# Optimization experiments

Measured on AMD Instinct MI355X. Metric: run time of the kernel, lower is better.

## Reference

```python
import jax, jax.numpy as jnp
import numpy as np

HEADS = 16
D_MODEL = 1024
D_K = D_MODEL // HEADS


def setup_inputs() -> dict:
    key = jax.random.key(0)
    ks = jax.random.split(key, 11)
    B, S, D = 4, 2048, D_MODEL
    q = jax.random.normal(ks[0], (B, S, D), dtype=jnp.float32)
    k = jax.random.normal(ks[1], (B, S, D), dtype=jnp.float32)
    v = jax.random.normal(ks[2], (B, S, D), dtype=jnp.float32)
    s = 1.0 / np.sqrt(D)
    Wq = jax.random.normal(ks[3], (D, D), dtype=jnp.float32) * s
    bq = jax.random.normal(ks[4], (D,), dtype=jnp.float32) * 0.01
    Wk = jax.random.normal(ks[5], (D, D), dtype=jnp.float32) * s
    bk = jax.random.normal(ks[6], (D,), dtype=jnp.float32) * 0.01
    Wv = jax.random.normal(ks[7], (D, D), dtype=jnp.float32) * s
    bv = jax.random.normal(ks[8], (D,), dtype=jnp.float32) * 0.01
    Wo = jax.random.normal(ks[9], (D, D), dtype=jnp.float32) * s
    bo = jax.random.normal(ks[10], (D,), dtype=jnp.float32) * 0.01
    return {"q": q, "k": k, "v": v, "Wq": Wq, "bq": bq, "Wk": Wk, "bk": bk,
            "Wv": Wv, "bv": bv, "Wo": Wo, "bo": bo}


def reference(q, k, v, Wq, bq, Wk, bk, Wv, bv, Wo, bo):
    B, Sq, D = q.shape
    Sk = k.shape[1]
    # Linear projections (torch Linear: x @ W.T + b)
    q_ = (q @ Wq.T + bq).reshape(B, Sq, HEADS, D_K).transpose(0, 2, 1, 3)  # [B,H,Sq,Dk]
    k_ = (k @ Wk.T + bk).reshape(B, Sk, HEADS, D_K).transpose(0, 2, 1, 3)  # [B,H,Sk,Dk]
    v_ = (v @ Wv.T + bv).reshape(B, Sk, HEADS, D_K).transpose(0, 2, 1, 3)  # [B,H,Sk,Dk]
    scores = jnp.einsum("bhqd,bhkd->bhqk", q_, k_) / jnp.sqrt(jnp.float32(D_K))
    attn = jax.nn.softmax(scores, axis=-1)
    ctx = jnp.einsum("bhqk,bhkd->bhqd", attn, v_)  # [B,H,Sq,Dk]
    concat = ctx.transpose(0, 2, 1, 3).reshape(B, Sq, D)
    # dropout p=0 -> identity (eval)
    return concat @ Wo.T + bo
```

## Files before the change

### kernel.cpp

```cpp
#include <hip/hip_runtime.h>
#include <hip/hip_bf16.h>
#include <stdint.h>

typedef unsigned short u16;
typedef __attribute__((ext_vector_type(8))) short bf16x8;
typedef __attribute__((ext_vector_type(4))) float f32x4;
typedef __attribute__((ext_vector_type(16))) float f32x16;
typedef __attribute__((ext_vector_type(4))) int i32x4;

#define BATCH 4
#define HEADS 16
#define SEQ   2048
#define DMODEL 1024
#define DK    64
#define QSCALE (0.125f * 1.44269504088896340736f)

__device__ __forceinline__ u16 f2bf(float f) {
  __hip_bfloat16 h = __float2bfloat16(f);
  return *reinterpret_cast<u16*>(&h);
}

__device__ __forceinline__ int cvtpk(float a, float b) {
  int r;
  asm("v_cvt_pk_bf16_f32 %0, %1, %2" : "=v"(r) : "v"(a), "v"(b));
  return r;
}

__device__ __forceinline__ void plswap(int& a, int& b) {
  asm volatile("v_permlane32_swap_b32 %0, %1" : "+v"(a), "+v"(b));
}

__device__ __forceinline__ void gload_lds16(const u16* g, u16* l) {
  __builtin_amdgcn_global_load_lds((const __attribute__((address_space(1))) void*)g,
                                   (__attribute__((address_space(3))) void*)l, 16, 0, 0);
}

__device__ __forceinline__ void sbar() {
  asm volatile("" ::: "memory");
  __builtin_amdgcn_s_barrier();
  __builtin_amdgcn_sched_barrier(0);
}
#define WAITV(N)                                              \
  do {                                                        \
    asm volatile("s_waitcnt vmcnt(" #N ")" ::: "memory");     \
    __builtin_amdgcn_sched_barrier(0);                        \
  } while (0)

__global__ void cvt_w(const float* __restrict__ w0, const float* __restrict__ w1,
                      const float* __restrict__ w2, const float* __restrict__ w3,
                      u16* __restrict__ o0, u16* __restrict__ o1,
                      u16* __restrict__ o2, u16* __restrict__ o3) {
  const int sel = blockIdx.y;
  long i = ((long)blockIdx.x * blockDim.x + threadIdx.x) * 8;
  const float* in = (sel == 0) ? w0 : (sel == 1) ? w1 : (sel == 2) ? w2 : w3;
  u16* out = (sel == 0) ? o0 : (sel == 1) ? o1 : (sel == 2) ? o2 : o3;
  float4 a = *(const float4*)(in + i);
  float4 b = *(const float4*)(in + i + 4);
  i32x4 pk;
  pk[0] = cvtpk(a.x, a.y); pk[1] = cvtpk(a.z, a.w);
  pk[2] = cvtpk(b.x, b.y); pk[3] = cvtpk(b.z, b.w);
  *(i32x4*)(out + i) = pk;
}

__global__ __launch_bounds__(256, 4)
void gemm97_qkv(const float* __restrict__ qf, const float* __restrict__ kf,
                const float* __restrict__ vf, const u16* __restrict__ Wqb,
                const u16* __restrict__ Wkb, const u16* __restrict__ Wvb,
                const float* __restrict__ bq, const float* __restrict__ bk,
                const float* __restrict__ bv, u16* __restrict__ Qp,
                u16* __restrict__ Kp, u16* __restrict__ Vt) {
  __shared__ __align__(16) u16 smem[16384];
  u16* As = smem;
  u16* Bs = smem + 8192;
  const int K = DMODEL;
  const int tid = threadIdx.x;
  const int lane = tid & 63;
  const int w = tid >> 6;
  const int wm = w >> 1, wn = w & 1;
  const int lr = lane & 15, lg = lane >> 4;

  const int wg = blockIdx.y * 24 + blockIdx.x;
  const int swz = (wg & 7) * 192 + (wg >> 3);
  const int bcolg = swz % 24;
  const int brow = swz / 24;
  const int sel = bcolg >> 3;
  const int bcol = bcolg & 7;

  const float* Ag = ((sel == 0) ? qf : (sel == 1) ? kf : vf) + (size_t)(brow * 128) * K;
  const u16* Bg = ((sel == 0) ? Wqb : (sel == 1) ? Wkb : Wvb) + (size_t)(bcol * 128) * K;
  const float* bias = (sel == 0) ? bq : (sel == 1) ? bk : bv;

  const int r0_ = tid >> 2;
  const int cc_ = (tid & 3) * 8;

  f32x4 acc[4][4] = {};
  float4 areg[2][2];

  areg[0][0] = *(const float4*)(Ag + (size_t)r0_ * K + cc_);
  areg[0][1] = *(const float4*)(Ag + (size_t)r0_ * K + cc_ + 4);
  areg[1][0] = *(const float4*)(Ag + (size_t)(r0_ + 64) * K + cc_);
  areg[1][1] = *(const float4*)(Ag + (size_t)(r0_ + 64) * K + cc_ + 4);
#pragma unroll
  for (int j = 0; j < 2; j++) {
    i32x4 pk;
    pk[0] = cvtpk(areg[j][0].x, areg[j][0].y);
    pk[1] = cvtpk(areg[j][0].z, areg[j][0].w);
    pk[2] = cvtpk(areg[j][1].x, areg[j][1].y);
    pk[3] = cvtpk(areg[j][1].z, areg[j][1].w);
    *(i32x4*)(As + (tid + j * 256) * 8) = pk;
  }
  gload_lds16(Bg + (size_t)r0_ * K + cc_, Bs + tid * 8);
  gload_lds16(Bg + (size_t)(r0_ + 64) * K + cc_, Bs + (tid + 256) * 8);
  areg[0][0] = *(const float4*)(Ag + (size_t)r0_ * K + 32 + cc_);
  areg[0][1] = *(const float4*)(Ag + (size_t)r0_ * K + 32 + cc_ + 4);
  areg[1][0] = *(const float4*)(Ag + (size_t)(r0_ + 64) * K + 32 + cc_);
  areg[1][1] = *(const float4*)(Ag + (size_t)(r0_ + 64) * K + 32 + cc_ + 4);
  __syncthreads();

  const int NT = 32;
  for (int t = 0; t < NT; ++t) {
    const int p = t & 1;
    const u16* Ab = As + p * 4096;
    const u16* Bb = Bs + p * 4096;

    if (t + 1 < NT) {
      u16* Ad = As + (p ^ 1) * 4096;
#pragma unroll
      for (int j = 0; j < 2; j++) {
        i32x4 pk;
        pk[0] = cvtpk(areg[j][0].x, areg[j][0].y);
        pk[1] = cvtpk(areg[j][0].z, areg[j][0].w);
        pk[2] = cvtpk(areg[j][1].x, areg[j][1].y);
        pk[3] = cvtpk(areg[j][1].z, areg[j][1].w);
        *(i32x4*)(Ad + (tid + j * 256) * 8) = pk;
      }
      u16* Bd = Bs + (p ^ 1) * 4096;
      const int k1 = (t + 1) * 32;
      gload_lds16(Bg + (size_t)r0_ * K + k1 + cc_, Bd + tid * 8);
      gload_lds16(Bg + (size_t)(r0_ + 64) * K + k1 + cc_, Bd + (tid + 256) * 8);
      if (t + 2 < NT) {
        const int k2 = (t + 2) * 32;
        areg[0][0] = *(const float4*)(Ag + (size_t)r0_ * K + k2 + cc_);
        areg[0][1] = *(const float4*)(Ag + (size_t)r0_ * K + k2 + cc_ + 4);
        areg[1][0] = *(const float4*)(Ag + (size_t)(r0_ + 64) * K + k2 + cc_);
        areg[1][1] = *(const float4*)(Ag + (size_t)(r0_ + 64) * K + k2 + cc_ + 4);
      }
    }

    bf16x8 a[4], b[4];
#pragma unroll
    for (int i = 0; i < 4; i++)
      a[i] = *(const bf16x8*)&Ab[(wm * 64 + i * 16 + lr) * 32 + lg * 8];
#pragma unroll
    for (int j = 0; j < 4; j++)
      b[j] = *(const bf16x8*)&Bb[(wn * 64 + j * 16 + lr) * 32 + lg * 8];
    __builtin_amdgcn_s_setprio(1);
#pragma unroll
    for (int i = 0; i < 4; i++)
#pragma unroll
      for (int j = 0; j < 4; j++)
        acc[i][j] = __builtin_amdgcn_mfma_f32_16x16x32_bf16(a[i], b[j], acc[i][j], 0, 0, 0);
    __builtin_amdgcn_s_setprio(0);

    __syncthreads();
  }

  if (sel < 2) {
    u16* Cout = (sel == 0) ? Qp : Kp;
    const float oscale = (sel == 0) ? QSCALE : 1.f;
#pragma unroll
    for (int j = 0; j < 4; j++) {
      const int col = bcol * 128 + wn * 64 + j * 16 + lr;
      const float bv_ = bias[col];
#pragma unroll
      for (int i = 0; i < 4; i++) {
        const int row0 = brow * 128 + wm * 64 + i * 16 + lg * 4;
#pragma unroll
        for (int r = 0; r < 4; r++)
          Cout[(size_t)(row0 + r) * DMODEL + col] = f2bf((acc[i][j][r] + bv_) * oscale);
      }
    }
  } else {
    const int b = brow >> 4;
    const int s0 = (brow & 15) * 128;
    u16* tr = smem;
    __syncthreads();
#pragma unroll
    for (int j = 0; j < 4; j++) {
      const int col = wn * 64 + j * 16 + lr;
      const int xsw = (col & 7) << 3;
      const float bv_ = bias[bcol * 128 + col];
#pragma unroll
      for (int i = 0; i < 4; i++) {
        const int rr0 = wm * 64 + i * 16 + lg * 4;
#pragma unroll
        for (int pr = 0; pr < 2; pr++) {
          const float e0 = acc[i][j][pr * 2] + bv_;
          const float e1 = acc[i][j][pr * 2 + 1] + bv_;
          *(int*)&tr[col * 128 + ((rr0 + pr * 2) ^ xsw)] = cvtpk(e0, e1);
        }
      }
    }
    __syncthreads();
    const int col = tid >> 1;
    const int part = tid & 1;
    const int xsw = (col & 7) << 3;
    const int c = bcol * 128 + col;
    const int hh = c >> 6, dk = c & 63;
    u16* dst = Vt + (size_t)((b * 16 + hh) * 64 + dk) * SEQ + s0 + part * 64;
#pragma unroll
    for (int jj = 0; jj < 8; jj++) {
      bf16x8 vv = *(const bf16x8*)&tr[col * 128 + ((part * 64 + jj * 8) ^ xsw)];
      *(bf16x8*)(dst + jj * 8) = vv;
    }
  }
}

__device__ __forceinline__ void gemm_kloop(
    const u16* __restrict__ Ag, const u16* __restrict__ Bg,
    u16* As, u16* Bs, f32x4 acc[4][4],
    const int tid, const int wm, const int wn, const int lr, const int lg) {
  const int K = DMODEL;
  int arow[4], acolc[4], brow2[2], bcol2[2];
#pragma unroll
  for (int j = 0; j < 4; j++) {
    const int c = tid + j * 512;
    arow[j] = c >> 3;
    acolc[j] = ((c & 7) ^ (arow[j] & 7)) * 8;
  }
#pragma unroll
  for (int j = 0; j < 2; j++) {
    const int c = tid + j * 512;
    brow2[j] = c >> 3;
    bcol2[j] = ((c & 7) ^ (brow2[j] & 7)) * 8;
  }

#pragma unroll
  for (int j = 0; j < 4; j++)
    gload_lds16(Ag + (size_t)arow[j] * K + acolc[j], As + (tid + j * 512) * 8);
#pragma unroll
  for (int j = 0; j < 2; j++)
    gload_lds16(Bg + (size_t)brow2[j] * K + bcol2[j], Bs + (tid + j * 512) * 8);
#pragma unroll
  for (int j = 0; j < 4; j++)
    gload_lds16(Ag + (size_t)arow[j] * K + 64 + acolc[j], As + 16384 + (tid + j * 512) * 8);
#pragma unroll
  for (int j = 0; j < 2; j++)
    gload_lds16(Bg + (size_t)brow2[j] * K + 64 + bcol2[j], Bs + 8192 + (tid + j * 512) * 8);
  WAITV(6);
  sbar();

  int m = 0;
  for (int t = 0; t < 16; ++t) {
    u16* Ab = As + m * 16384;
    u16* Bb = Bs + (t & 1) * 8192;
    const int m2 = (m + 2 >= 3) ? m - 1 : m + 2;
    const int k1 = (t + 1) * 64;
    const int k2 = (t + 2) * 64;

    bf16x8 a[4], b[4];
#pragma unroll
    for (int i = 0; i < 4; i++) {
      const int r = wm * 64 + i * 16 + lr;
      a[i] = *(const bf16x8*)&Ab[r * 64 + ((lg ^ (r & 7)) * 8)];
    }
#pragma unroll
    for (int j = 0; j < 4; j++) {
      const int r = wn * 64 + j * 16 + lr;
      b[j] = *(const bf16x8*)&Bb[r * 64 + ((lg ^ (r & 7)) * 8)];
    }
    if (t + 1 < 16) {
      u16* Bd = Bs + ((t + 1) & 1) * 8192;
      gload_lds16(Bg + (size_t)brow2[0] * K + k1 + bcol2[0], Bd + tid * 8);
      gload_lds16(Bg + (size_t)brow2[1] * K + k1 + bcol2[1], Bd + (tid + 512) * 8);
    }
    if (t + 2 < 16) {
      u16* Ad = As + m2 * 16384;
      gload_lds16(Ag + (size_t)arow[0] * K + k2 + acolc[0], Ad + tid * 8);
      gload_lds16(Ag + (size_t)arow[1] * K + k2 + acolc[1], Ad + (tid + 512) * 8);
    }
    sbar();
    __builtin_amdgcn_s_setprio(1);
#pragma unroll
    for (int i = 0; i < 4; i++)
#pragma unroll
      for (int j = 0; j < 4; j++)
        acc[i][j] = __builtin_amdgcn_mfma_f32_16x16x32_bf16(a[i], b[j], acc[i][j], 0, 0, 0);
    __builtin_amdgcn_s_setprio(0);
    sbar();

#pragma unroll
    for (int i = 0; i < 4; i++) {
      const int r = wm * 64 + i * 16 + lr;
      a[i] = *(const bf16x8*)&Ab[r * 64 + (((4 + lg) ^ (r & 7)) * 8)];
    }
#pragma unroll
    for (int j = 0; j < 4; j++) {
      const int r = wn * 64 + j * 16 + lr;
      b[j] = *(const bf16x8*)&Bb[r * 64 + (((4 + lg) ^ (r & 7)) * 8)];
    }
    if (t + 2 < 16) {
      u16* Ad = As + m2 * 16384;
      gload_lds16(Ag + (size_t)arow[2] * K + k2 + acolc[2], Ad + (tid + 1024) * 8);
      gload_lds16(Ag + (size_t)arow[3] * K + k2 + acolc[3], Ad + (tid + 1536) * 8);
    }
    sbar();
    __builtin_amdgcn_s_setprio(1);
#pragma unroll
    for (int i = 0; i < 4; i++)
#pragma unroll
      for (int j = 0; j < 4; j++)
        acc[i][j] = __builtin_amdgcn_mfma_f32_16x16x32_bf16(a[i], b[j], acc[i][j], 0, 0, 0);
    __builtin_amdgcn_s_setprio(0);
    if (t < 14) {
      WAITV(4);
    } else {
      WAITV(0);
    }
    sbar();
    m = (m + 1 >= 3) ? 0 : m + 1;
  }
}

__global__ __launch_bounds__(512, 2)
void gemm8_bt(const u16* __restrict__ A, const u16* __restrict__ Bm,
              const float* __restrict__ bias, float* __restrict__ Cout) {
  __shared__ __align__(16) u16 smem[65536];
  u16* As = smem;
  u16* Bs = smem + 49152;
  const int tid = threadIdx.x;
  const int lane = tid & 63;
  const int w = tid >> 6;
  const int wm = w >> 1, wn = w & 1;
  const int lr = lane & 15, lg = lane >> 4;

  const int wg = blockIdx.y * 8 + blockIdx.x;
  const int swz = (wg & 7) * 32 + (wg >> 3);
  const int bcol = swz & 7;
  const int brow = swz >> 3;

  f32x4 acc[4][4] = {};
  gemm_kloop(A + (size_t)(brow * 256) * DMODEL, Bm + (size_t)(bcol * 128) * DMODEL,
             As, Bs, acc, tid, wm, wn, lr, lg);

#pragma unroll
  for (int j = 0; j < 4; j++) {
    const int col = bcol * 128 + wn * 64 + j * 16 + lr;
    const float bv_ = bias[col];
#pragma unroll
    for (int i = 0; i < 4; i++) {
      const int row0 = brow * 256 + wm * 64 + i * 16 + lg * 4;
#pragma unroll
      for (int r = 0; r < 4; r++)
        Cout[(size_t)(row0 + r) * DMODEL + col] = acc[i][j][r] + bv_;
    }
  }
}

__device__ __forceinline__ void pack_group(const float* p, int* pw) {
  int W0 = cvtpk(p[0], p[1]);
  int W1 = cvtpk(p[2], p[3]);
  int W2 = cvtpk(p[4], p[5]);
  int W3 = cvtpk(p[6], p[7]);
  plswap(W0, W2);
  plswap(W1, W3);
  pw[0] = W0; pw[1] = W1; pw[2] = W2; pw[3] = W3;
}

__global__ __launch_bounds__(256, 4)
void attn2(const u16* __restrict__ Qp, const u16* __restrict__ Kp,
           const u16* __restrict__ Vt, u16* __restrict__ ctx) {
  __shared__ __align__(16) u16 smem[16384];
  const int tid = threadIdx.x;
  const int lane = tid & 63, w = tid >> 6;
  const int hi = lane >> 5;
  const int l31 = lane & 31;

  const int wg = blockIdx.y * gridDim.x + blockIdx.x;
  const int swz = (wg & 7) * 128 + (wg >> 3);
  const int bh = swz >> 4;
  const int b = bh >> 4, h = bh & 15;
  const int q0 = (swz & 15) * 128 + w * 32;

  const u16* qrow = Qp + (size_t)(b * SEQ + q0 + l31) * DMODEL + h * DK + hi * 8;
  bf16x8 qf[4];
#pragma unroll
  for (int kk = 0; kk < 4; kk++) qf[kk] = *(const bf16x8*)(qrow + kk * 16);

  const int srow = tid >> 3;
  const int scb = tid & 7;
  const int scol = (scb ^ (srow & 7)) * 8;
  const u16* kp = Kp + (size_t)(b * SEQ + srow) * DMODEL + h * DK + scol;
  const u16* vp = Vt + (size_t)bh * DK * SEQ + (size_t)srow * SEQ + scol;

  const int ksw = (l31 & 7) << 3;

  f32x16 o0 = {}, o1 = {};
  float lacc[4] = {};
  const int NT = SEQ / 64;

  {
    u16* Kd = smem;
    u16* Vd = smem + 4096;
    gload_lds16(kp, Kd + tid * 8);
    gload_lds16(kp + 32 * DMODEL, Kd + tid * 8 + 2048);
    gload_lds16(vp, Vd + tid * 8);
    gload_lds16(vp + 32 * SEQ, Vd + tid * 8 + 2048);
    kp += 64 * DMODEL;
    vp += 64;
  }
  __syncthreads();

  for (int t = 0; t < NT; ++t) {
    const int p = t & 1;
    if (t + 1 < NT) {
      u16* Kd = smem + ((p ^ 1) << 13);
      u16* Vd = Kd + 4096;
      gload_lds16(kp, Kd + tid * 8);
      gload_lds16(kp + 32 * DMODEL, Kd + tid * 8 + 2048);
      gload_lds16(vp, Vd + tid * 8);
      gload_lds16(vp + 32 * SEQ, Vd + tid * 8 + 2048);
      kp += 64 * DMODEL;
      vp += 64;
    }

    const u16* Kc = smem + (p << 13);
    const u16* Vc = Kc + 4096;

    f32x16 st0 = {}, st1 = {};
    __builtin_amdgcn_s_setprio(1);
#pragma unroll
    for (int kk = 0; kk < 4; kk++) {
      const int slot = (((kk * 2 + hi) << 3) ^ ksw);
      bf16x8 k0 = *(const bf16x8*)&Kc[l31 * 64 + slot];
      bf16x8 k1 = *(const bf16x8*)&Kc[(l31 + 32) * 64 + slot];
      st0 = __builtin_amdgcn_mfma_f32_32x32x16_bf16(k0, qf[kk], st0, 0, 0, 0);
      st1 = __builtin_amdgcn_mfma_f32_32x32x16_bf16(k1, qf[kk], st1, 0, 0, 0);
    }
    __builtin_amdgcn_s_setprio(0);

#pragma unroll
    for (int i = 0; i < 16; i++) st0[i] = __builtin_amdgcn_exp2f(st0[i]);
#pragma unroll
    for (int i = 0; i < 16; i++) st1[i] = __builtin_amdgcn_exp2f(st1[i]);
    float ts[8];
#pragma unroll
    for (int i = 0; i < 8; i++) ts[i] = (st0[i] + st0[i + 8]) + (st1[i] + st1[i + 8]);
#pragma unroll
    for (int i = 0; i < 4; i++) lacc[i] += ts[i] + ts[i + 4];

    int pw[4][4];
    {
      float tmp[8];
#pragma unroll
      for (int i = 0; i < 8; i++) tmp[i] = st0[i];
      pack_group(tmp, pw[0]);
#pragma unroll
      for (int i = 0; i < 8; i++) tmp[i] = st0[i + 8];
      pack_group(tmp, pw[1]);
#pragma unroll
      for (int i = 0; i < 8; i++) tmp[i] = st1[i];
      pack_group(tmp, pw[2]);
#pragma unroll
      for (int i = 0; i < 8; i++) tmp[i] = st1[i + 8];
      pack_group(tmp, pw[3]);
    }

    __builtin_amdgcn_s_setprio(1);
#pragma unroll
    for (int c = 0; c < 4; c++) {
      i32x4 pwv;
      pwv[0] = pw[c][0]; pwv[1] = pw[c][1]; pwv[2] = pw[c][2]; pwv[3] = pw[c][3];
      bf16x8 pf = __builtin_bit_cast(bf16x8, pwv);
      const int slot = (((c * 2 + hi) << 3) ^ ksw);
      bf16x8 v0 = *(const bf16x8*)&Vc[l31 * 64 + slot];
      bf16x8 v1 = *(const bf16x8*)&Vc[(l31 + 32) * 64 + slot];
      o0 = __builtin_amdgcn_mfma_f32_32x32x16_bf16(v0, pf, o0, 0, 0, 0);
      o1 = __builtin_amdgcn_mfma_f32_32x32x16_bf16(v1, pf, o1, 0, 0, 0);
    }
    __builtin_amdgcn_s_setprio(0);

    __syncthreads();
  }

  float lsum = (lacc[0] + lacc[1]) + (lacc[2] + lacc[3]);
  lsum += __shfl_xor(lsum, 32);
  const float rl = 1.0f / lsum;
  u16* ot = smem + w * (32 * 72);
#pragma unroll
  for (int ds_ = 0; ds_ < 2; ds_++) {
#pragma unroll
    for (int g = 0; g < 4; g++) {
#pragma unroll
      for (int pr = 0; pr < 2; pr++) {
        const int r = g * 4 + pr * 2;
        const int d = ds_ * 32 + (r & 3) + 8 * (r >> 2) + 4 * hi;
        float e0 = (ds_ ? o1[r] : o0[r]) * rl;
        float e1 = (ds_ ? o1[r + 1] : o0[r + 1]) * rl;
        *(int*)&ot[l31 * 72 + d] = cvtpk(e0, e1);
      }
    }
  }
  __syncthreads();
  const int rq = lane >> 3;
  const int rc = (lane & 7) * 8;
#pragma unroll
  for (int it = 0; it < 4; ++it) {
    const int qq = it * 8 + rq;
    bf16x8 vrow = *(const bf16x8*)&ot[qq * 72 + rc];
    *(bf16x8*)&ctx[(size_t)(b * SEQ + q0 + qq) * DMODEL + h * DK + rc] = vrow;
  }
}

extern "C" void kernel_launch(void* const* d_in, const int* in_sizes, int n_in,
                              void* d_out, int out_size, void* d_ws, size_t ws_size,
                              hipStream_t stream) {
  const float* q  = (const float*)d_in[0];
  const float* k  = (const float*)d_in[1];
  const float* v  = (const float*)d_in[2];
  const float* Wq = (const float*)d_in[3];
  const float* bq = (const float*)d_in[4];
  const float* Wk = (const float*)d_in[5];
  const float* bk = (const float*)d_in[6];
  const float* Wv = (const float*)d_in[7];
  const float* bv = (const float*)d_in[8];
  const float* Wo = (const float*)d_in[9];
  const float* bo = (const float*)d_in[10];

  char* ws = (char*)d_ws;
  const size_t MB = 1024 * 1024;
  u16* Wqb = (u16*)(ws + 48 * MB);
  u16* Wkb = (u16*)(ws + 50 * MB);
  u16* Wvb = (u16*)(ws + 52 * MB);
  u16* Wob = (u16*)(ws + 54 * MB);
  u16* Qp  = (u16*)(ws + 56 * MB);
  u16* Kp  = (u16*)(ws + 72 * MB);
  u16* Vt  = (u16*)(ws + 104 * MB);
  u16* ctx = (u16*)(ws + 120 * MB);

  const long nW = (long)DMODEL * DMODEL;

  cvt_w<<<dim3(nW / 8 / 256, 4), 256, 0, stream>>>(Wq, Wk, Wv, Wo, Wqb, Wkb, Wvb, Wob);

  gemm97_qkv<<<dim3(24, 64), 256, 0, stream>>>(q, k, v, Wqb, Wkb, Wvb,
                                               bq, bk, bv, Qp, Kp, Vt);

  attn2<<<dim3(16, 64), 256, 0, stream>>>(Qp, Kp, Vt, ctx);

  gemm8_bt<<<dim3(8, 32), 512, 0, stream>>>(ctx, Wob, bo, (float*)d_out);
}
```

Before: 188.9 us.

## Triple-buffer weight tiles and XOR-swizzle LDS layout in QKV projection GEMM

Weight (B) tiles in the QKV projection GEMM move from double to triple buffering, so global-to-LDS loads are issued two iterations ahead. The __syncthreads at the end of each iteration is replaced by explicit vmcnt/lgkmcnt waits plus a barrier. The LDS column chunks are XOR-swizzled by row to reduce bank conflicts on the fragment reads. The cost is more LDS per block, which may reduce occupancy at 4 blocks per CU, plus fragile hand-counted waitcnt values.

```diff
diff --git a/kernel.cpp b/kernel.cpp
--- a/kernel.cpp
+++ b/kernel.cpp
@@ -43,6 +43,11 @@
 #define WAITV(N)                                              \
   do {                                                        \
     asm volatile("s_waitcnt vmcnt(" #N ")" ::: "memory");     \
+    __builtin_amdgcn_sched_barrier(0);                        \
+  } while (0)
+#define WAITLGKM0()                                           \
+  do {                                                        \
+    asm volatile("s_waitcnt lgkmcnt(0)" ::: "memory");        \
     __builtin_amdgcn_sched_barrier(0);                        \
   } while (0)
 
@@ -69,7 +74,7 @@
                 const float* __restrict__ bq, const float* __restrict__ bk,
                 const float* __restrict__ bv, u16* __restrict__ Qp,
                 u16* __restrict__ Kp, u16* __restrict__ Vt) {
-  __shared__ __align__(16) u16 smem[16384];
+  __shared__ __align__(16) u16 smem[20480];
   u16* As = smem;
   u16* Bs = smem + 8192;
   const int K = DMODEL;
@@ -91,15 +96,16 @@
   const float* bias = (sel == 0) ? bq : (sel == 1) ? bk : bv;
 
   const int r0_ = tid >> 2;
-  const int cc_ = (tid & 3) * 8;
+  const int c0_ = (((tid & 3) ^ (r0_ & 3)) * 8);
+  const int c1_ = (((tid & 3) ^ ((r0_ + 64) & 3)) * 8);
 
   f32x4 acc[4][4] = {};
   float4 areg[2][2];
 
-  areg[0][0] = *(const float4*)(Ag + (size_t)r0_ * K + cc_);
-  areg[0][1] = *(const float4*)(Ag + (size_t)r0_ * K + cc_ + 4);
-  areg[1][0] = *(const float4*)(Ag + (size_t)(r0_ + 64) * K + cc_);
-  areg[1][1] = *(const float4*)(Ag + (size_t)(r0_ + 64) * K + cc_ + 4);
+  areg[0][0] = *(const float4*)(Ag + (size_t)r0_ * K + c0_);
+  areg[0][1] = *(const float4*)(Ag + (size_t)r0_ * K + c0_ + 4);
+  areg[1][0] = *(const float4*)(Ag + (size_t)(r0_ + 64) * K + c1_);
+  areg[1][1] = *(const float4*)(Ag + (size_t)(r0_ + 64) * K + c1_ + 4);
 #pragma unroll
   for (int j = 0; j < 2; j++) {
     i32x4 pk;
@@ -109,19 +115,24 @@
     pk[3] = cvtpk(areg[j][1].z, areg[j][1].w);
     *(i32x4*)(As + (tid + j * 256) * 8) = pk;
   }
-  gload_lds16(Bg + (size_t)r0_ * K + cc_, Bs + tid * 8);
-  gload_lds16(Bg + (size_t)(r0_ + 64) * K + cc_, Bs + (tid + 256) * 8);
-  areg[0][0] = *(const float4*)(Ag + (size_t)r0_ * K + 32 + cc_);
-  areg[0][1] = *(const float4*)(Ag + (size_t)r0_ * K + 32 + cc_ + 4);
-  areg[1][0] = *(const float4*)(Ag + (size_t)(r0_ + 64) * K + 32 + cc_);
-  areg[1][1] = *(const float4*)(Ag + (size_t)(r0_ + 64) * K + 32 + cc_ + 4);
-  __syncthreads();
+  gload_lds16(Bg + (size_t)r0_ * K + c0_, Bs + tid * 8);
+  gload_lds16(Bg + (size_t)(r0_ + 64) * K + c1_, Bs + (tid + 256) * 8);
+  gload_lds16(Bg + (size_t)r0_ * K + 32 + c0_, Bs + 4096 + tid * 8);
+  gload_lds16(Bg + (size_t)(r0_ + 64) * K + 32 + c1_, Bs + 4096 + (tid + 256) * 8);
+  areg[0][0] = *(const float4*)(Ag + (size_t)r0_ * K + 32 + c0_);
+  areg[0][1] = *(const float4*)(Ag + (size_t)r0_ * K + 32 + c0_ + 4);
+  areg[1][0] = *(const float4*)(Ag + (size_t)(r0_ + 64) * K + 32 + c1_);
+  areg[1][1] = *(const float4*)(Ag + (size_t)(r0_ + 64) * K + 32 + c1_ + 4);
+  WAITV(6);
+  WAITLGKM0();
+  sbar();
 
   const int NT = 32;
+  int bcur = 0;
   for (int t = 0; t < NT; ++t) {
     const int p = t & 1;
     const u16* Ab = As + p * 4096;
-    const u16* Bb = Bs + p * 4096;
+    const u16* Bb = Bs + bcur * 4096;
 
     if (t + 1 < NT) {
       u16* Ad = As + (p ^ 1) * 4096;
@@ -134,26 +145,31 @@
         pk[3] = cvtpk(areg[j][1].z, areg[j][1].w);
         *(i32x4*)(Ad + (tid + j * 256) * 8) = pk;
       }
-      u16* Bd = Bs + (p ^ 1) * 4096;
-      const int k1 = (t + 1) * 32;
-      gload_lds16(Bg + (size_t)r0_ * K + k1 + cc_, Bd + tid * 8);
-      gload_lds16(Bg + (size_t)(r0_ + 64) * K + k1 + cc_, Bd + (tid + 256) * 8);
       if (t + 2 < NT) {
         const int k2 = (t + 2) * 32;
-        areg[0][0] = *(const float4*)(Ag + (size_t)r0_ * K + k2 + cc_);
-        areg[0][1] = *(const float4*)(Ag + (size_t)r0_ * K + k2 + cc_ + 4);
-        areg[1][0] = *(const float4*)(Ag + (size_t)(r0_ + 64) * K + k2 + cc_);
-        areg[1][1] = *(const float4*)(Ag + (size_t)(r0_ + 64) * K + k2 + cc_ + 4);
+        areg[0][0] = *(const float4*)(Ag + (size_t)r0_ * K + k2 + c0_);
+        areg[0][1] = *(const float4*)(Ag + (size_t)r0_ * K + k2 + c0_ + 4);
+        areg[1][0] = *(const float4*)(Ag + (size_t)(r0_ + 64) * K + k2 + c1_);
+        areg[1][1] = *(const float4*)(Ag + (size_t)(r0_ + 64) * K + k2 + c1_ + 4);
+        const int bn2 = (bcur + 2 >= 3) ? bcur - 1 : bcur + 2;
+        u16* Bd = Bs + bn2 * 4096;
+        gload_lds16(Bg + (size_t)r0_ * K + k2 + c0_, Bd + tid * 8);
+        gload_lds16(Bg + (size_t)(r0_ + 64) * K + k2 + c1_, Bd + (tid + 256) * 8);
       }
+      __builtin_amdgcn_sched_barrier(0);
     }
 
     bf16x8 a[4], b[4];
 #pragma unroll
-    for (int i = 0; i < 4; i++)
-      a[i] = *(const bf16x8*)&Ab[(wm * 64 + i * 16 + lr) * 32 + lg * 8];
-#pragma unroll
-    for (int j = 0; j < 4; j++)
-      b[j] = *(const bf16x8*)&Bb[(wn * 64 + j * 16 + lr) * 32 + lg * 8];
+    for (int i = 0; i < 4; i++) {
+      const int r = wm * 64 + i * 16 + lr;
+      a[i] = *(const bf16x8*)&Ab[r * 32 + ((lg ^ (r & 3)) * 8)];
+    }
+#pragma unroll
+    for (int j = 0; j < 4; j++) {
+      const int r = wn * 64 + j * 16 + lr;
+      b[j] = *(const bf16x8*)&Bb[r * 32 + ((lg ^ (r & 3)) * 8)];
+    }
     __builtin_amdgcn_s_setprio(1);
 #pragma unroll
     for (int i = 0; i < 4; i++)
@@ -162,7 +178,14 @@
         acc[i][j] = __builtin_amdgcn_mfma_f32_16x16x32_bf16(a[i], b[j], acc[i][j], 0, 0, 0);
     __builtin_amdgcn_s_setprio(0);
 
-    __syncthreads();
+    if (t + 2 < NT) {
+      WAITV(6);
+    } else {
+      WAITV(0);
+    }
+    WAITLGKM0();
+    sbar();
+    bcur = (bcur + 1 >= 3) ? 0 : bcur + 1;
   }
 
   if (sel < 2) {
```

Result: no change. 189.0 us (median of 2 runs) (+0.0%).
